# Performance work log

Hardware: AMD Instinct MI355X
Metric: run time of the kernel (lower is better)

Reference implementation:

```python
import jax, jax.numpy as jnp
import numpy as np

# config constants
B, S, H = 4, 2048, 1024
E = 8                 # n_routed_experts
M = 512               # moe_intermediate_size
K = 2                 # num_experts_per_tok
N_SHARED = 2
SM = M * N_SHARED     # shared expert intermediate
G = 64                # gene_size
GE_TEMP = 1.0
ALPHA = 0.001         # aux_loss_alpha
SEQ_AUX = True
NORM_TOPK = True
COS_TEMP = 0.78
CONS_ALPHA = 0.01
LEAKY_SLOPE = 0.01
EPS_COS = 1e-8


def setup_inputs() -> dict:
    key = jax.random.key(0)
    ks = jax.random.split(key, 12)
    sh = 1.0 / np.sqrt(H)
    sm = 1.0 / np.sqrt(M)
    ssm = 1.0 / np.sqrt(SM)
    sg = 1.0 / np.sqrt(G)
    return {
        "hidden_states": jax.random.normal(ks[0], (B, S, H), jnp.float32),
        "g": jax.random.normal(ks[1], (B, G), jnp.float32),
        "wt": jax.random.uniform(ks[2], (E, H), jnp.float32, -sh, sh),   # gate weight_token
        "wg": jax.random.uniform(ks[3], (E, G), jnp.float32, -sg, sg),   # gate weight_gene
        "w_gate": jax.random.uniform(ks[4], (E, H, M), jnp.float32, -sh, sh),
        "w_up": jax.random.uniform(ks[5], (E, H, M), jnp.float32, -sh, sh),
        "w_down": jax.random.uniform(ks[6], (E, M, H), jnp.float32, -sm, sm),
        "sw_gate": jax.random.uniform(ks[7], (H, SM), jnp.float32, -sh, sh),
        "sw_up": jax.random.uniform(ks[8], (H, SM), jnp.float32, -sh, sh),
        "sw_down": jax.random.uniform(ks[9], (SM, H), jnp.float32, -ssm, ssm),
    }


def _leaky(x):
    return jnp.where(x >= 0, x, LEAKY_SLOPE * x)


def _moe_forward(hidden_states, g, wt, wg, w_gate, w_up, w_down, sw_gate, sw_up, sw_down):
    b, s, h = hidden_states.shape
    x = hidden_states.reshape(-1, h)                    # [T, H], T = b*s
    T = x.shape[0]

    # ---- gate ----
    logits_h = x @ wt.T                                 # [T, E]
    logits_g = g @ wg.T                                 # [b, E]
    logits_g = jnp.repeat(logits_g, s, axis=0)          # [T, E]
    logits = (logits_h + logits_g / GE_TEMP) / (1.0 + 1.0 / GE_TEMP)
    scores = jax.nn.softmax(logits, axis=-1)            # [T, E]
    topk_w, topk_idx = jax.lax.top_k(scores, K)         # [T, K]
    if K > 1 and NORM_TOPK:
        topk_w = topk_w / (topk_w.sum(-1, keepdims=True) + 1e-20)

    # aux loss (seq_aux=True)
    onehot = jax.nn.one_hot(topk_idx.reshape(b, s * K), E, dtype=jnp.float32)  # [b, s*K, E]
    ce = onehot.sum(1) / (s * K / E)                    # [b, E]
    aux_loss = (ce * scores.reshape(b, s, E).mean(1)).sum(1).mean() * ALPHA

    # ---- routed experts: dense stacked compute, then gather ----
    gp = _leaky(jnp.einsum('th,ehm->etm', x, w_gate))   # [E, T, M]
    up = jnp.einsum('th,ehm->etm', x, w_up)
    y_all = jnp.einsum('etm,emh->eth', gp * up, w_down) # [E, T, H]
    y_sel = y_all[topk_idx, jnp.arange(T)[:, None], :]  # [T, K, H]
    y = (y_sel * topk_w[..., None]).sum(1).reshape(b, s, h)

    # ---- shared expert ----
    p = (_leaky(hidden_states @ sw_gate) * (hidden_states @ sw_up)) @ sw_down
    y = y + p

    # consistency cosine loss
    num = jnp.sum(y * p, -1)
    den = jnp.maximum(jnp.linalg.norm(y, axis=-1), EPS_COS) * jnp.maximum(jnp.linalg.norm(p, axis=-1), EPS_COS)
    closs = CONS_ALPHA * jnp.mean((num / den) / (1.0 + COS_TEMP))
    return y, aux_loss + closs


def reference(hidden_states, g, wt, wg, w_gate, w_up, w_down, sw_gate, sw_up, sw_down):
    y, _ = _moe_forward(hidden_states, g, wt, wg, w_gate, w_up, w_down, sw_gate, sw_up, sw_down)
    return y
```

## Files before the change

### kernel.cpp

```cpp
#include <hip/hip_runtime.h>
#include <stdint.h>

#define T_TOK 8192
#define H_DIM 1024
#define M_DIM 512
#define SM_DIM 1024
#define E_NUM 8
#define S_SEQ 2048
#define G_DIM 64
#define NASSIGN 16384
#define NSLOT (NASSIGN + E_NUM * 256)
#define MAX_TILES (NASSIGN / 256 + E_NUM)
#define NBLK_PLACE (NASSIGN / 256)

typedef float f32x4 __attribute__((ext_vector_type(4)));
typedef short bf16x8 __attribute__((ext_vector_type(8)));

struct TileDesc { int base; int expert; int nrows; };

#define WAITCNT_VM4 asm volatile("s_waitcnt vmcnt(4)" ::: "memory")
#define WAITCNT_VM3 asm volatile("s_waitcnt vmcnt(3)" ::: "memory")
#define WAITCNT_VM0 asm volatile("s_waitcnt vmcnt(0)" ::: "memory")
#define WAITCNT_LGKM0 asm volatile("s_waitcnt lgkmcnt(0)" ::: "memory")

static __device__ __forceinline__ ushort f2b(float f) {
  union { float f; uint32_t u; } a; a.f = f;
  uint32_t r = a.u + 0x7fffu + ((a.u >> 16) & 1u);
  return (ushort)(r >> 16);
}
static __device__ __forceinline__ float b2f(ushort u) {
  union { uint32_t u; float f; } a; a.u = ((uint32_t)u) << 16;
  return a.f;
}
static __device__ __forceinline__ int imin(int a, int b) { return a < b ? a : b; }

static __device__ __forceinline__ void gll16(const void* g, void* l) {
  __builtin_amdgcn_global_load_lds(
      (const __attribute__((address_space(1))) void*)g,
      (__attribute__((address_space(3))) void*)l, 16, 0, 0);
}
static __device__ __forceinline__ int swz(int row) { return (row >> 1) & 3; }
static __device__ __forceinline__ int xcd_remap(int wg, int nwg) {
  return (wg & 7) * (nwg >> 3) + (wg >> 3);
}

__global__ void cvt_x_kernel(const float* __restrict__ x, ushort* __restrict__ xb) {
  int i = blockIdx.x * 256 + threadIdx.x;
  const float4 v = ((const float4*)x)[i];
  ushort4 o;
  o.x = f2b(v.x); o.y = f2b(v.y); o.z = f2b(v.z); o.w = f2b(v.w);
  ((ushort4*)xb)[i] = o;
}

__global__ void tcvt_kernel(const float* __restrict__ src, ushort* __restrict__ dst, int R, int C) {
  __shared__ float tile[32][33];
  size_t bo = (size_t)blockIdx.z * R * C;
  src += bo; dst += bo;
  int c0 = blockIdx.x * 32, r0 = blockIdx.y * 32;
#pragma unroll
  for (int i = 0; i < 4; ++i)
    tile[threadIdx.y + i * 8][threadIdx.x] =
        src[(size_t)(r0 + threadIdx.y + i * 8) * C + c0 + threadIdx.x];
  __syncthreads();
#pragma unroll
  for (int i = 0; i < 4; ++i)
    dst[(size_t)(c0 + threadIdx.y + i * 8) * R + r0 + threadIdx.x] =
        f2b(tile[threadIdx.x][threadIdx.y + i * 8]);
}

__global__ void lg_kernel(const float* __restrict__ g, const float* __restrict__ wg,
                          float* __restrict__ lg) {
  int tid = threadIdx.x;
  if (tid < 4 * E_NUM) {
    int b = tid >> 3, e = tid & 7;
    float s = 0.f;
    for (int i = 0; i < G_DIM; ++i) s += g[b * G_DIM + i] * wg[e * G_DIM + i];
    lg[tid] = s;
  }
}

__global__ __launch_bounds__(64) void router_kernel(
    const float* __restrict__ x, const float* __restrict__ wt, const float* __restrict__ lg,
    int* __restrict__ tidx, float* __restrict__ tw) {
  int t = blockIdx.x;
  int lane = threadIdx.x;
  const float* xr = x + (size_t)t * H_DIM;
  float a[E_NUM];
#pragma unroll
  for (int e = 0; e < E_NUM; ++e) a[e] = 0.f;
  for (int i = lane; i < H_DIM; i += 64) {
    float xv = xr[i];
#pragma unroll
    for (int e = 0; e < E_NUM; ++e) a[e] += xv * wt[e * H_DIM + i];
  }
#pragma unroll
  for (int e = 0; e < E_NUM; ++e)
    for (int off = 32; off; off >>= 1) a[e] += __shfl_xor(a[e], off, 64);
  if (lane == 0) {
    int b = t / S_SEQ;
    float l[E_NUM];
#pragma unroll
    for (int e = 0; e < E_NUM; ++e) l[e] = 0.5f * (a[e] + lg[b * E_NUM + e]);
    int i1 = 0; float b1 = l[0];
#pragma unroll
    for (int e = 1; e < E_NUM; ++e) if (l[e] > b1) { b1 = l[e]; i1 = e; }
    int i2 = -1; float b2 = -1e30f;
#pragma unroll
    for (int e = 0; e < E_NUM; ++e) if (e != i1 && l[e] > b2) { b2 = l[e]; i2 = e; }
    float e2 = expf(b2 - b1);
    float inv = 1.f / (1.f + e2);
    tidx[t * 2] = i1; tidx[t * 2 + 1] = i2;
    tw[t * 2] = inv;  tw[t * 2 + 1] = e2 * inv;
  }
}

__global__ __launch_bounds__(256) void hist_kernel(const int* __restrict__ tidx,
                                                   int* __restrict__ bcount) {
  __shared__ int h[E_NUM];
  int tid = threadIdx.x;
  if (tid < E_NUM) h[tid] = 0;
  __syncthreads();
  atomicAdd(&h[tidx[blockIdx.x * 256 + tid]], 1);
  __syncthreads();
  if (tid < E_NUM) bcount[blockIdx.x * E_NUM + tid] = h[tid];
}

__global__ __launch_bounds__(64) void scan2_kernel(
    const int* __restrict__ bcount, int* __restrict__ boffs, int* __restrict__ offs,
    TileDesc* __restrict__ desc, int* __restrict__ ndesc) {
  __shared__ int cnt[E_NUM];
  __shared__ int off_s[E_NUM];
  int lane = threadIdx.x;
  if (lane < E_NUM) {
    int s = 0;
    for (int b = 0; b < NBLK_PLACE; ++b) s += bcount[b * E_NUM + lane];
    cnt[lane] = s;
  }
  __syncthreads();
  if (lane == 0) {
    int o = 0, nd = 0;
    for (int e = 0; e < E_NUM; ++e) {
      off_s[e] = o;
      offs[e] = o;
      int n = cnt[e];
      for (int tb = 0; tb < n; tb += 256) {
        desc[nd].base = o + tb; desc[nd].expert = e;
        desc[nd].nrows = imin(n - tb, 256);
        ++nd;
      }
      o += n;
    }
    offs[E_NUM] = o;
    *ndesc = nd;
  }
  __syncthreads();
  if (lane < E_NUM) {
    int run = off_s[lane];
    for (int b = 0; b < NBLK_PLACE; ++b) {
      boffs[b * E_NUM + lane] = run;
      run += bcount[b * E_NUM + lane];
    }
  }
}

__global__ __launch_bounds__(256) void place2_kernel(
    const int* __restrict__ tidx, const int* __restrict__ boffs,
    int* __restrict__ perm, int* __restrict__ slot_of) {
  __shared__ int wcnt[4][E_NUM];
  int tid = threadIdx.x, wv = tid >> 6, lane = tid & 63;
  int i = blockIdx.x * 256 + tid;
  int e = tidx[i];
  unsigned long long lower = (lane == 63) ? 0x7fffffffffffffffull : ((1ull << lane) - 1ull);
  int rank = 0;
#pragma unroll
  for (int ee = 0; ee < E_NUM; ++ee) {
    unsigned long long m = __ballot(e == ee);
    if (e == ee) rank = __popcll(m & lower);
    if (lane == 0) wcnt[wv][ee] = __popcll(m);
  }
  __syncthreads();
  int off = boffs[blockIdx.x * E_NUM + e];
  for (int w = 0; w < wv; ++w) off += wcnt[w][e];
  int pos = off + rank;
  perm[pos] = i >> 1;
  slot_of[i] = pos;
}

template <int DUAL>
static __device__ __forceinline__ void gemm_core(
    const ushort* __restrict__ A, const ushort* __restrict__ B0,
    const ushort* __restrict__ B1, void* __restrict__ Out, int outf32,
    int Kd, int NdOut, int rowbase, int nrows, int n0,
    const int* __restrict__ perm, ushort* Asb, ushort* Bsb) {
  constexpr int BN = DUAL ? 256 : 128;
  constexpr int BSTRIDE = BN * 32;
  int tid = threadIdx.x, wv = tid >> 6, lane = tid & 63;
  int sr = tid >> 2, sc = tid & 3;
  int r1 = sr + 128;

  int ga0 = perm ? perm[rowbase + imin(sr, nrows - 1)] : (rowbase + sr);
  int ga1 = perm ? perm[rowbase + imin(r1, nrows - 1)] : (rowbase + r1);
  const ushort* ap0 = A + (size_t)ga0 * Kd + ((sc ^ swz(sr)) << 3);
  const ushort* ap1 = A + (size_t)ga1 * Kd + ((sc ^ swz(r1)) << 3);
  const ushort* bp0;
  const ushort* bp1 = nullptr;
  if (DUAL) {
    int rb0 = n0 + sr, rb1 = n0 + r1;
    const ushort* s0 = ((rb0 >> 4) & 1) ? B1 : B0;
    const ushort* s1 = ((rb1 >> 4) & 1) ? B1 : B0;
    bp0 = s0 + (size_t)(((rb0 >> 5) << 4) + (rb0 & 15)) * Kd + ((sc ^ swz(sr)) << 3);
    bp1 = s1 + (size_t)(((rb1 >> 5) << 4) + (rb1 & 15)) * Kd + ((sc ^ swz(r1)) << 3);
  } else {
    bp0 = B0 + (size_t)(n0 + sr) * Kd + ((sc ^ swz(sr)) << 3);
  }

  auto stageA = [&](int b) {
    ushort* ad = Asb + b * 8192 + wv * 512;
    gll16(ap0, ad); gll16(ap1, ad + 4096);
    ap0 += 32; ap1 += 32;
  };
  auto stageB = [&](int b) {
    ushort* bd = Bsb + b * BSTRIDE + wv * 512;
    gll16(bp0, bd); bp0 += 32;
    if (DUAL) { gll16(bp1, bd + 4096); bp1 += 32; }
  };

  int wr = wv >> 2, wc = wv & 3;
  int lr = lane & 15, cg = lane >> 4;

  constexpr int NF = DUAL ? 4 : 2;
  f32x4 acc[8][NF];
#pragma unroll
  for (int m = 0; m < 8; ++m)
#pragma unroll
    for (int n = 0; n < NF; ++n) acc[m][n] = (f32x4){0.f, 0.f, 0.f, 0.f};

  int nk = Kd >> 5;
  stageA(0); stageB(0);
  stageA(1); stageB(1);
  if (DUAL) WAITCNT_VM4; else WAITCNT_VM3;
  __builtin_amdgcn_s_barrier();

  for (int kt = 0; kt < nk; ++kt) {
    int b = kt % 3;
    const ushort* abuf = Asb + b * 8192;
    const ushort* bbuf = Bsb + b * BSTRIDE;
    bool pf = (kt + 2 < nk);
    int b2 = (kt + 2) % 3;

    if (DUAL) {
      bf16x8 af[8];
#pragma unroll
      for (int m = 0; m < 8; ++m) {
        int row = wr * 128 + m * 16 + lr;
        af[m] = *(const bf16x8*)(abuf + row * 32 + ((cg ^ swz(row)) << 3));
      }
      bf16x8 bq[2];
#pragma unroll
      for (int n = 0; n < 2; ++n) {
        int row = wc * 64 + n * 16 + lr;
        bq[n] = *(const bf16x8*)(bbuf + row * 32 + ((cg ^ swz(row)) << 3));
      }
      if (pf) stageA(b2);
      __builtin_amdgcn_s_setprio(1);
#pragma unroll
      for (int m = 0; m < 8; ++m) {
        acc[m][0] = __builtin_amdgcn_mfma_f32_16x16x32_bf16(af[m], bq[0], acc[m][0], 0, 0, 0);
        acc[m][1] = __builtin_amdgcn_mfma_f32_16x16x32_bf16(af[m], bq[1], acc[m][1], 0, 0, 0);
      }
      __builtin_amdgcn_s_setprio(0);
      bf16x8 bq2[2];
#pragma unroll
      for (int n = 0; n < 2; ++n) {
        int row = wc * 64 + (n + 2) * 16 + lr;
        bq2[n] = *(const bf16x8*)(bbuf + row * 32 + ((cg ^ swz(row)) << 3));
      }
      if (pf) stageB(b2);
      __builtin_amdgcn_s_setprio(1);
#pragma unroll
      for (int m = 0; m < 8; ++m) {
        acc[m][2] = __builtin_amdgcn_mfma_f32_16x16x32_bf16(af[m], bq2[0], acc[m][2], 0, 0, 0);
        acc[m][3] = __builtin_amdgcn_mfma_f32_16x16x32_bf16(af[m], bq2[1], acc[m][3], 0, 0, 0);
      }
      __builtin_amdgcn_s_setprio(0);
    } else {
      bf16x8 bq[2];
#pragma unroll
      for (int n = 0; n < 2; ++n) {
        int row = wc * 32 + n * 16 + lr;
        bq[n] = *(const bf16x8*)(bbuf + row * 32 + ((cg ^ swz(row)) << 3));
      }
      bf16x8 af[4];
#pragma unroll
      for (int m = 0; m < 4; ++m) {
        int row = wr * 128 + m * 16 + lr;
        af[m] = *(const bf16x8*)(abuf + row * 32 + ((cg ^ swz(row)) << 3));
      }
      if (pf) { stageA(b2); stageB(b2); }
      __builtin_amdgcn_s_setprio(1);
#pragma unroll
      for (int m = 0; m < 4; ++m) {
        acc[m][0] = __builtin_amdgcn_mfma_f32_16x16x32_bf16(af[m], bq[0], acc[m][0], 0, 0, 0);
        acc[m][1] = __builtin_amdgcn_mfma_f32_16x16x32_bf16(af[m], bq[1], acc[m][1], 0, 0, 0);
      }
      __builtin_amdgcn_s_setprio(0);
      bf16x8 af2[4];
#pragma unroll
      for (int m = 0; m < 4; ++m) {
        int row = wr * 128 + (m + 4) * 16 + lr;
        af2[m] = *(const bf16x8*)(abuf + row * 32 + ((cg ^ swz(row)) << 3));
      }
      __builtin_amdgcn_s_setprio(1);
#pragma unroll
      for (int m = 0; m < 4; ++m) {
        acc[m + 4][0] = __builtin_amdgcn_mfma_f32_16x16x32_bf16(af2[m], bq[0], acc[m + 4][0], 0, 0, 0);
        acc[m + 4][1] = __builtin_amdgcn_mfma_f32_16x16x32_bf16(af2[m], bq[1], acc[m + 4][1], 0, 0, 0);
      }
      __builtin_amdgcn_s_setprio(0);
    }
    WAITCNT_LGKM0;
    if (pf) { if (DUAL) WAITCNT_VM4; else WAITCNT_VM3; }
    else WAITCNT_VM0;
    __builtin_amdgcn_s_barrier();
  }

  int rq = cg * 4, cq = lr;
  if (DUAL) {
#pragma unroll
    for (int m = 0; m < 8; ++m)
#pragma unroll
      for (int p = 0; p < 2; ++p)
#pragma unroll
        for (int r = 0; r < 4; ++r) {
          int row = wr * 128 + m * 16 + rq + r;
          if (row < nrows) {
            float gv = acc[m][2 * p][r], uv = acc[m][2 * p + 1][r];
            float hv = (gv >= 0.f ? gv : 0.01f * gv) * uv;
            int col = (n0 >> 1) + wc * 32 + p * 16 + cq;
            ((ushort*)Out)[(size_t)(rowbase + row) * NdOut + col] = f2b(hv);
          }
        }
  } else {
#pragma unroll
    for (int m = 0; m < 8; ++m)
#pragma unroll
      for (int n = 0; n < 2; ++n)
#pragma unroll
        for (int r = 0; r < 4; ++r) {
          int row = wr * 128 + m * 16 + rq + r;
          if (row < nrows) {
            int col = n0 + wc * 32 + n * 16 + cq;
            size_t o = (size_t)(rowbase + row) * NdOut + col;
            if (outf32) ((float*)Out)[o] = acc[m][n][r];
            else ((ushort*)Out)[o] = f2b(acc[m][n][r]);
          }
        }
  }
}

__global__ __launch_bounds__(512) void gemm_dual_all(
    const ushort* __restrict__ xb, const ushort* __restrict__ swg,
    const ushort* __restrict__ swu, ushort* __restrict__ hsh,
    const ushort* __restrict__ wg, const ushort* __restrict__ wu,
    ushort* __restrict__ h_e, const int* __restrict__ perm,
    const TileDesc* __restrict__ desc, const int* __restrict__ ndesc) {
  __shared__ ushort Asb[3 * 8192];
  __shared__ ushort Bsb[3 * 8192];
  int id = xcd_remap(blockIdx.x, gridDim.x);
  if (id < 256) {
    int mt = id >> 3, n0 = (id & 7) * 256;
    gemm_core<1>(xb, swg, swu, hsh, 0, H_DIM, SM_DIM, mt * 256, 256, n0, nullptr, Asb, Bsb);
  } else {
    int rid = id - 256;
    int mt = rid >> 2, n0 = (rid & 3) * 256;
    if (mt >= *ndesc) return;
    TileDesc d = desc[mt];
    size_t wo = (size_t)d.expert * M_DIM * H_DIM;
    gemm_core<1>(xb, wg + wo, wu + wo, h_e, 0, H_DIM, M_DIM, d.base, d.nrows, n0, perm, Asb, Bsb);
  }
}

__global__ __launch_bounds__(512) void gemm_down_all(
    const ushort* __restrict__ hsh, const ushort* __restrict__ swd, float* __restrict__ y,
    const ushort* __restrict__ h_e, const ushort* __restrict__ wd, ushort* __restrict__ ye,
    const TileDesc* __restrict__ desc, const int* __restrict__ ndesc) {
  __shared__ ushort Asb[3 * 8192];
  __shared__ ushort Bsb[3 * 4096];
  int id = xcd_remap(blockIdx.x, gridDim.x);
  if (id < 256) {
    int mt = id >> 3, n0 = (id & 7) * 128;
    gemm_core<0>(hsh, swd, nullptr, (void*)y, 1, SM_DIM, H_DIM, mt * 256, 256, n0, nullptr, Asb, Bsb);
  } else {
    int rid = id - 256;
    int mt = rid >> 3, n0 = (rid & 7) * 128;
    if (mt >= *ndesc) return;
    TileDesc d = desc[mt];
    gemm_core<0>(h_e, wd + (size_t)d.expert * H_DIM * M_DIM, nullptr, (void*)ye, 0,
                 M_DIM, H_DIM, d.base, d.nrows, n0, nullptr, Asb, Bsb);
  }
}

__global__ void final_kernel(float* __restrict__ y, const ushort* __restrict__ ye,
                             const int* __restrict__ slot_of, const float* __restrict__ tw) {
  int i = blockIdx.x * 256 + threadIdx.x;
  int t = i >> 8;
  int c4 = (i & 255) * 4;
  int s0 = slot_of[t * 2], s1 = slot_of[t * 2 + 1];
  float w0 = tw[t * 2], w1 = tw[t * 2 + 1];
  float4 v = ((float4*)y)[i];
  ushort4 a = *(const ushort4*)(ye + (size_t)s0 * H_DIM + c4);
  ushort4 b = *(const ushort4*)(ye + (size_t)s1 * H_DIM + c4);
  v.x += w0 * b2f(a.x) + w1 * b2f(b.x);
  v.y += w0 * b2f(a.y) + w1 * b2f(b.y);
  v.z += w0 * b2f(a.z) + w1 * b2f(b.z);
  v.w += w0 * b2f(a.w) + w1 * b2f(b.w);
  ((float4*)y)[i] = v;
}

extern "C" void kernel_launch(void* const* d_in, const int* in_sizes, int n_in,
                              void* d_out, int out_size, void* d_ws, size_t ws_size,
                              hipStream_t stream) {
  const float* x       = (const float*)d_in[0];
  const float* g       = (const float*)d_in[1];
  const float* wt      = (const float*)d_in[2];
  const float* wg      = (const float*)d_in[3];
  const float* w_gate  = (const float*)d_in[4];
  const float* w_up    = (const float*)d_in[5];
  const float* w_down  = (const float*)d_in[6];
  const float* sw_gate = (const float*)d_in[7];
  const float* sw_up   = (const float*)d_in[8];
  const float* sw_down = (const float*)d_in[9];
  float* y = (float*)d_out;

  char* p = (char*)d_ws;
  auto alloc = [&](size_t bytes) -> char* {
    char* r = p;
    p += (bytes + 255) & ~(size_t)255;
    return r;
  };
  ushort* xb    = (ushort*)alloc((size_t)T_TOK * H_DIM * 2);
  ushort* wg_t  = (ushort*)alloc((size_t)E_NUM * M_DIM * H_DIM * 2);
  ushort* wu_t  = (ushort*)alloc((size_t)E_NUM * M_DIM * H_DIM * 2);
  ushort* wd_t  = (ushort*)alloc((size_t)E_NUM * H_DIM * M_DIM * 2);
  ushort* swg_t = (ushort*)alloc((size_t)SM_DIM * H_DIM * 2);
  ushort* swu_t = (ushort*)alloc((size_t)SM_DIM * H_DIM * 2);
  ushort* swd_t = (ushort*)alloc((size_t)H_DIM * SM_DIM * 2);
  float* lg     = (float*)alloc(4 * E_NUM * 4);
  int* tidx     = (int*)alloc(NASSIGN * 4);
  float* tw     = (float*)alloc(NASSIGN * 4);
  int* bcount   = (int*)alloc(NBLK_PLACE * E_NUM * 4);
  int* boffs    = (int*)alloc(NBLK_PLACE * E_NUM * 4);
  int* offs     = (int*)alloc((E_NUM + 1) * 4);
  int* ndesc    = (int*)alloc(4);
  int* perm     = (int*)alloc(NASSIGN * 4);
  int* slot_of  = (int*)alloc(NASSIGN * 4);
  TileDesc* desc = (TileDesc*)alloc(MAX_TILES * sizeof(TileDesc));
  ushort* h_e   = (ushort*)alloc((size_t)NSLOT * M_DIM * 2);
  ushort* hsh   = (ushort*)alloc((size_t)T_TOK * SM_DIM * 2);
  ushort* ye    = (ushort*)alloc((size_t)NSLOT * H_DIM * 2);
  (void)ws_size; (void)in_sizes; (void)n_in; (void)out_size;

  cvt_x_kernel<<<T_TOK * H_DIM / 4 / 256, 256, 0, stream>>>(x, xb);
  dim3 tb(32, 8);
  tcvt_kernel<<<dim3(M_DIM / 32, H_DIM / 32, E_NUM), tb, 0, stream>>>(w_gate, wg_t, H_DIM, M_DIM);
  tcvt_kernel<<<dim3(M_DIM / 32, H_DIM / 32, E_NUM), tb, 0, stream>>>(w_up, wu_t, H_DIM, M_DIM);
  tcvt_kernel<<<dim3(H_DIM / 32, M_DIM / 32, E_NUM), tb, 0, stream>>>(w_down, wd_t, M_DIM, H_DIM);
  tcvt_kernel<<<dim3(SM_DIM / 32, H_DIM / 32, 1), tb, 0, stream>>>(sw_gate, swg_t, H_DIM, SM_DIM);
  tcvt_kernel<<<dim3(SM_DIM / 32, H_DIM / 32, 1), tb, 0, stream>>>(sw_up, swu_t, H_DIM, SM_DIM);
  tcvt_kernel<<<dim3(H_DIM / 32, SM_DIM / 32, 1), tb, 0, stream>>>(sw_down, swd_t, SM_DIM, H_DIM);

  lg_kernel<<<1, 32, 0, stream>>>(g, wg, lg);
  router_kernel<<<T_TOK, 64, 0, stream>>>(x, wt, lg, tidx, tw);
  hist_kernel<<<NBLK_PLACE, 256, 0, stream>>>(tidx, bcount);
  scan2_kernel<<<1, 64, 0, stream>>>(bcount, boffs, offs, desc, ndesc);
  place2_kernel<<<NBLK_PLACE, 256, 0, stream>>>(tidx, boffs, perm, slot_of);

  gemm_dual_all<<<256 + MAX_TILES * 4, 512, 0, stream>>>(
      xb, swg_t, swu_t, hsh, wg_t, wu_t, h_e, perm, desc, ndesc);
  gemm_down_all<<<256 + MAX_TILES * 8, 512, 0, stream>>>(
      hsh, swd_t, y, h_e, wd_t, ye, desc, ndesc);

  final_kernel<<<T_TOK * H_DIM / 4 / 256, 256, 0, stream>>>(y, ye, slot_of, tw);
}
```

Measured before the change: 233.3 us.

## Rewrite GEMM core as 256x256 tile with BK=64 quadrant-pipelined double buffer

Replaces the triple-buffered BK=32 GEMM core with a double-buffered BK=64 core that splits the 256x256 tile into four 128x128 quadrants. Loads for the next K-step are issued between quadrant MFMA phases, each phase separated by a barrier. The down-projection now also uses 256-wide N tiles, halving its grid and doubling reuse of each A tile. The intent is fewer barriers per unit of K, more compute per load, and better overlap of global-to-LDS traffic. The cost is 128KB of LDS per block, which limits occupancy to one block per CU, plus four barriers per K-step.

After: 222.2 us. -4.7%, faster.

```diff
diff --git a/kernel.cpp b/kernel.cpp
--- a/kernel.cpp
+++ b/kernel.cpp
@@ -18,8 +18,9 @@
 
 struct TileDesc { int base; int expert; int nrows; };
 
+#define WAITCNT_VM6 asm volatile("s_waitcnt vmcnt(6)" ::: "memory")
 #define WAITCNT_VM4 asm volatile("s_waitcnt vmcnt(4)" ::: "memory")
-#define WAITCNT_VM3 asm volatile("s_waitcnt vmcnt(3)" ::: "memory")
+#define WAITCNT_VM2 asm volatile("s_waitcnt vmcnt(2)" ::: "memory")
 #define WAITCNT_VM0 asm volatile("s_waitcnt vmcnt(0)" ::: "memory")
 #define WAITCNT_LGKM0 asm volatile("s_waitcnt lgkmcnt(0)" ::: "memory")
 
@@ -39,7 +40,6 @@
       (const __attribute__((address_space(1))) void*)g,
       (__attribute__((address_space(3))) void*)l, 16, 0, 0);
 }
-static __device__ __forceinline__ int swz(int row) { return (row >> 1) & 3; }
 static __device__ __forceinline__ int xcd_remap(int wg, int nwg) {
   return (wg & 7) * (nwg >> 3) + (wg >> 3);
 }
@@ -187,175 +187,175 @@
 }
 
 template <int DUAL>
-static __device__ __forceinline__ void gemm_core(
+static __device__ __forceinline__ void gemm_core8(
     const ushort* __restrict__ A, const ushort* __restrict__ B0,
     const ushort* __restrict__ B1, void* __restrict__ Out, int outf32,
     int Kd, int NdOut, int rowbase, int nrows, int n0,
-    const int* __restrict__ perm, ushort* Asb, ushort* Bsb) {
-  constexpr int BN = DUAL ? 256 : 128;
-  constexpr int BSTRIDE = BN * 32;
+    const int* __restrict__ perm, ushort* __restrict__ LDS) {
   int tid = threadIdx.x, wv = tid >> 6, lane = tid & 63;
-  int sr = tid >> 2, sc = tid & 3;
-  int r1 = sr + 128;
-
-  int ga0 = perm ? perm[rowbase + imin(sr, nrows - 1)] : (rowbase + sr);
-  int ga1 = perm ? perm[rowbase + imin(r1, nrows - 1)] : (rowbase + r1);
-  const ushort* ap0 = A + (size_t)ga0 * Kd + ((sc ^ swz(sr)) << 3);
-  const ushort* ap1 = A + (size_t)ga1 * Kd + ((sc ^ swz(r1)) << 3);
-  const ushort* bp0;
-  const ushort* bp1 = nullptr;
-  if (DUAL) {
-    int rb0 = n0 + sr, rb1 = n0 + r1;
-    const ushort* s0 = ((rb0 >> 4) & 1) ? B1 : B0;
-    const ushort* s1 = ((rb1 >> 4) & 1) ? B1 : B0;
-    bp0 = s0 + (size_t)(((rb0 >> 5) << 4) + (rb0 & 15)) * Kd + ((sc ^ swz(sr)) << 3);
-    bp1 = s1 + (size_t)(((rb1 >> 5) << 4) + (rb1 & 15)) * Kd + ((sc ^ swz(r1)) << 3);
-  } else {
-    bp0 = B0 + (size_t)(n0 + sr) * Kd + ((sc ^ swz(sr)) << 3);
-  }
-
-  auto stageA = [&](int b) {
-    ushort* ad = Asb + b * 8192 + wv * 512;
-    gll16(ap0, ad); gll16(ap1, ad + 4096);
-    ap0 += 32; ap1 += 32;
-  };
-  auto stageB = [&](int b) {
-    ushort* bd = Bsb + b * BSTRIDE + wv * 512;
-    gll16(bp0, bd); bp0 += 32;
-    if (DUAL) { gll16(bp1, bd + 4096); bp1 += 32; }
-  };
-
   int wr = wv >> 2, wc = wv & 3;
   int lr = lane & 15, cg = lane >> 4;
-
-  constexpr int NF = DUAL ? 4 : 2;
-  f32x4 acc[8][NF];
-#pragma unroll
-  for (int m = 0; m < 8; ++m)
-#pragma unroll
-    for (int n = 0; n < NF; ++n) acc[m][n] = (f32x4){0.f, 0.f, 0.f, 0.f};
-
-  int nk = Kd >> 5;
-  stageA(0); stageB(0);
-  stageA(1); stageB(1);
-  if (DUAL) WAITCNT_VM4; else WAITCNT_VM3;
+  int sid = lane >> 3, dch = lane & 7;
+
+  const ushort* apA[2][2];
+  const ushort* apB[2][2];
+#pragma unroll
+  for (int qm = 0; qm < 2; ++qm)
+#pragma unroll
+    for (int k = 0; k < 2; ++k) {
+      int idx = k * 64 + wv * 8 + sid;
+      int gch = dch ^ (idx & 7);
+      int grow = (idx >> 6) * 128 + qm * 64 + (idx & 63);
+      grow = imin(grow, nrows - 1);
+      int arow = perm ? perm[rowbase + grow] : rowbase + grow;
+      apA[qm][k] = A + (size_t)arow * Kd + gch * 8;
+    }
+#pragma unroll
+  for (int qn = 0; qn < 2; ++qn)
+#pragma unroll
+    for (int k = 0; k < 2; ++k) {
+      int idx = k * 64 + wv * 8 + sid;
+      int gch = dch ^ (idx & 7);
+      int vrow = n0 + (idx >> 5) * 64 + qn * 32 + (idx & 31);
+      const ushort* src; int brow;
+      if (DUAL) {
+        src = ((vrow >> 4) & 1) ? B1 : B0;
+        brow = (vrow >> 5) * 16 + (vrow & 15);
+      } else {
+        src = B0; brow = vrow;
+      }
+      apB[qn][k] = src + (size_t)brow * Kd + gch * 8;
+    }
+
+  auto stgA = [&](int qm, int k, int nd) {
+    gll16(apA[qm][k], LDS + nd * 16384 + qm * 8192 + (k * 512 + wv * 64) * 8);
+    apA[qm][k] += 64;
+  };
+  auto stgB = [&](int qn, int k, int nd) {
+    gll16(apB[qn][k], LDS + 32768 + nd * 16384 + qn * 8192 + (k * 512 + wv * 64) * 8);
+    apB[qn][k] += 64;
+  };
+  auto rdA = [&](int d, int qm, int m, int kk) -> bf16x8 {
+    int idx = wr * 64 + m * 16 + lr;
+    int ch = (kk * 4 + cg) ^ (idx & 7);
+    return *(const bf16x8*)(LDS + d * 16384 + qm * 8192 + idx * 64 + ch * 8);
+  };
+  auto rdB = [&](int d, int qn, int n, int kk) -> bf16x8 {
+    int idx = wc * 32 + n * 16 + lr;
+    int ch = (kk * 4 + cg) ^ (idx & 7);
+    return *(const bf16x8*)(LDS + 32768 + d * 16384 + qn * 8192 + idx * 64 + ch * 8);
+  };
+
+  f32x4 acc[2][2][4][2];
+#pragma unroll
+  for (int qm = 0; qm < 2; ++qm)
+#pragma unroll
+    for (int qn = 0; qn < 2; ++qn)
+#pragma unroll
+      for (int m = 0; m < 4; ++m)
+#pragma unroll
+        for (int n = 0; n < 2; ++n) acc[qm][qn][m][n] = (f32x4){0.f, 0.f, 0.f, 0.f};
+
+  int nk = Kd >> 6;
+  stgA(0, 0, 0); stgA(0, 1, 0);
+  stgB(0, 0, 0); stgB(0, 1, 0);
+  stgB(1, 0, 0); stgB(1, 1, 0);
+  stgA(1, 0, 0); stgA(1, 1, 0);
+  WAITCNT_VM4;
   __builtin_amdgcn_s_barrier();
 
-  for (int kt = 0; kt < nk; ++kt) {
-    int b = kt % 3;
-    const ushort* abuf = Asb + b * 8192;
-    const ushort* bbuf = Bsb + b * BSTRIDE;
-    bool pf = (kt + 2 < nk);
-    int b2 = (kt + 2) % 3;
-
-    if (DUAL) {
-      bf16x8 af[8];
-#pragma unroll
-      for (int m = 0; m < 8; ++m) {
-        int row = wr * 128 + m * 16 + lr;
-        af[m] = *(const bf16x8*)(abuf + row * 32 + ((cg ^ swz(row)) << 3));
-      }
-      bf16x8 bq[2];
+  for (int t = 0; t < nk; ++t) {
+    int cur = t & 1, nxt = cur ^ 1;
+    bool hn = (t + 1 < nk);
+    bf16x8 a0f[4][2], a1f[4][2], b0f[2][2], b1f[2][2];
+
+#pragma unroll
+    for (int m = 0; m < 4; ++m) { a0f[m][0] = rdA(cur, 0, m, 0); a0f[m][1] = rdA(cur, 0, m, 1); }
+#pragma unroll
+    for (int n = 0; n < 2; ++n) { b0f[n][0] = rdB(cur, 0, n, 0); b0f[n][1] = rdB(cur, 0, n, 1); }
+    if (hn) { stgA(0, 0, nxt); stgA(0, 1, nxt); WAITCNT_VM4; } else { WAITCNT_VM2; }
+    WAITCNT_LGKM0;
+    __builtin_amdgcn_s_barrier();
+    __builtin_amdgcn_s_setprio(1);
+#pragma unroll
+    for (int m = 0; m < 4; ++m)
 #pragma unroll
       for (int n = 0; n < 2; ++n) {
-        int row = wc * 64 + n * 16 + lr;
-        bq[n] = *(const bf16x8*)(bbuf + row * 32 + ((cg ^ swz(row)) << 3));
-      }
-      if (pf) stageA(b2);
-      __builtin_amdgcn_s_setprio(1);
-#pragma unroll
-      for (int m = 0; m < 8; ++m) {
-        acc[m][0] = __builtin_amdgcn_mfma_f32_16x16x32_bf16(af[m], bq[0], acc[m][0], 0, 0, 0);
-        acc[m][1] = __builtin_amdgcn_mfma_f32_16x16x32_bf16(af[m], bq[1], acc[m][1], 0, 0, 0);
-      }
-      __builtin_amdgcn_s_setprio(0);
-      bf16x8 bq2[2];
+        acc[0][0][m][n] = __builtin_amdgcn_mfma_f32_16x16x32_bf16(a0f[m][0], b0f[n][0], acc[0][0][m][n], 0, 0, 0);
+        acc[0][0][m][n] = __builtin_amdgcn_mfma_f32_16x16x32_bf16(a0f[m][1], b0f[n][1], acc[0][0][m][n], 0, 0, 0);
+      }
+    __builtin_amdgcn_s_setprio(0);
+
+#pragma unroll
+    for (int n = 0; n < 2; ++n) { b1f[n][0] = rdB(cur, 1, n, 0); b1f[n][1] = rdB(cur, 1, n, 1); }
+    if (hn) { stgB(0, 0, nxt); stgB(0, 1, nxt); WAITCNT_VM4; } else { WAITCNT_VM0; }
+    WAITCNT_LGKM0;
+    __builtin_amdgcn_s_barrier();
+    __builtin_amdgcn_s_setprio(1);
+#pragma unroll
+    for (int m = 0; m < 4; ++m)
 #pragma unroll
       for (int n = 0; n < 2; ++n) {
-        int row = wc * 64 + (n + 2) * 16 + lr;
-        bq2[n] = *(const bf16x8*)(bbuf + row * 32 + ((cg ^ swz(row)) << 3));
-      }
-      if (pf) stageB(b2);
-      __builtin_amdgcn_s_setprio(1);
-#pragma unroll
-      for (int m = 0; m < 8; ++m) {
-        acc[m][2] = __builtin_amdgcn_mfma_f32_16x16x32_bf16(af[m], bq2[0], acc[m][2], 0, 0, 0);
-        acc[m][3] = __builtin_amdgcn_mfma_f32_16x16x32_bf16(af[m], bq2[1], acc[m][3], 0, 0, 0);
-      }
-      __builtin_amdgcn_s_setprio(0);
-    } else {
-      bf16x8 bq[2];
+        acc[0][1][m][n] = __builtin_amdgcn_mfma_f32_16x16x32_bf16(a0f[m][0], b1f[n][0], acc[0][1][m][n], 0, 0, 0);
+        acc[0][1][m][n] = __builtin_amdgcn_mfma_f32_16x16x32_bf16(a0f[m][1], b1f[n][1], acc[0][1][m][n], 0, 0, 0);
+      }
+    __builtin_amdgcn_s_setprio(0);
+
+#pragma unroll
+    for (int m = 0; m < 4; ++m) { a1f[m][0] = rdA(cur, 1, m, 0); a1f[m][1] = rdA(cur, 1, m, 1); }
+    if (hn) { stgB(1, 0, nxt); stgB(1, 1, nxt); WAITCNT_VM6; }
+    WAITCNT_LGKM0;
+    __builtin_amdgcn_s_barrier();
+    __builtin_amdgcn_s_setprio(1);
+#pragma unroll
+    for (int m = 0; m < 4; ++m)
 #pragma unroll
       for (int n = 0; n < 2; ++n) {
-        int row = wc * 32 + n * 16 + lr;
-        bq[n] = *(const bf16x8*)(bbuf + row * 32 + ((cg ^ swz(row)) << 3));
-      }
-      bf16x8 af[4];
-#pragma unroll
-      for (int m = 0; m < 4; ++m) {
-        int row = wr * 128 + m * 16 + lr;
-        af[m] = *(const bf16x8*)(abuf + row * 32 + ((cg ^ swz(row)) << 3));
-      }
-      if (pf) { stageA(b2); stageB(b2); }
-      __builtin_amdgcn_s_setprio(1);
-#pragma unroll
-      for (int m = 0; m < 4; ++m) {
-        acc[m][0] = __builtin_amdgcn_mfma_f32_16x16x32_bf16(af[m], bq[0], acc[m][0], 0, 0, 0);
-        acc[m][1] = __builtin_amdgcn_mfma_f32_16x16x32_bf16(af[m], bq[1], acc[m][1], 0, 0, 0);
-      }
-      __builtin_amdgcn_s_setprio(0);
-      bf16x8 af2[4];
-#pragma unroll
-      for (int m = 0; m < 4; ++m) {
-        int row = wr * 128 + (m + 4) * 16 + lr;
-        af2[m] = *(const bf16x8*)(abuf + row * 32 + ((cg ^ swz(row)) << 3));
-      }
-      __builtin_amdgcn_s_setprio(1);
-#pragma unroll
-      for (int m = 0; m < 4; ++m) {
-        acc[m + 4][0] = __builtin_amdgcn_mfma_f32_16x16x32_bf16(af2[m], bq[0], acc[m + 4][0], 0, 0, 0);
-        acc[m + 4][1] = __builtin_amdgcn_mfma_f32_16x16x32_bf16(af2[m], bq[1], acc[m + 4][1], 0, 0, 0);
-      }
-      __builtin_amdgcn_s_setprio(0);
-    }
+        acc[1][0][m][n] = __builtin_amdgcn_mfma_f32_16x16x32_bf16(a1f[m][0], b0f[n][0], acc[1][0][m][n], 0, 0, 0);
+        acc[1][0][m][n] = __builtin_amdgcn_mfma_f32_16x16x32_bf16(a1f[m][1], b0f[n][1], acc[1][0][m][n], 0, 0, 0);
+      }
+    __builtin_amdgcn_s_setprio(0);
+
+    if (hn) { stgA(1, 0, nxt); stgA(1, 1, nxt); WAITCNT_VM4; }
     WAITCNT_LGKM0;
-    if (pf) { if (DUAL) WAITCNT_VM4; else WAITCNT_VM3; }
-    else WAITCNT_VM0;
     __builtin_amdgcn_s_barrier();
-  }
-
-  int rq = cg * 4, cq = lr;
-  if (DUAL) {
-#pragma unroll
-    for (int m = 0; m < 8; ++m)
-#pragma unroll
-      for (int p = 0; p < 2; ++p)
+    __builtin_amdgcn_s_setprio(1);
+#pragma unroll
+    for (int m = 0; m < 4; ++m)
+#pragma unroll
+      for (int n = 0; n < 2; ++n) {
+        acc[1][1][m][n] = __builtin_amdgcn_mfma_f32_16x16x32_bf16(a1f[m][0], b1f[n][0], acc[1][1][m][n], 0, 0, 0);
+        acc[1][1][m][n] = __builtin_amdgcn_mfma_f32_16x16x32_bf16(a1f[m][1], b1f[n][1], acc[1][1][m][n], 0, 0, 0);
+      }
+    __builtin_amdgcn_s_setprio(0);
+  }
+
+#pragma unroll
+  for (int qm = 0; qm < 2; ++qm)
+#pragma unroll
+    for (int qn = 0; qn < 2; ++qn)
+#pragma unroll
+      for (int m = 0; m < 4; ++m)
 #pragma unroll
         for (int r = 0; r < 4; ++r) {
-          int row = wr * 128 + m * 16 + rq + r;
+          int row = wr * 128 + qm * 64 + m * 16 + cg * 4 + r;
           if (row < nrows) {
-            float gv = acc[m][2 * p][r], uv = acc[m][2 * p + 1][r];
-            float hv = (gv >= 0.f ? gv : 0.01f * gv) * uv;
-            int col = (n0 >> 1) + wc * 32 + p * 16 + cq;
-            ((ushort*)Out)[(size_t)(rowbase + row) * NdOut + col] = f2b(hv);
+            if (DUAL) {
+              float gv = acc[qm][qn][m][0][r], uv = acc[qm][qn][m][1][r];
+              float hv = (gv >= 0.f ? gv : 0.01f * gv) * uv;
+              int col = ((n0 >> 5) + wc * 2 + qn) * 16 + lr;
+              ((ushort*)Out)[(size_t)(rowbase + row) * NdOut + col] = f2b(hv);
+            } else {
+#pragma unroll
+              for (int n = 0; n < 2; ++n) {
+                int col = n0 + wc * 64 + qn * 32 + n * 16 + lr;
+                size_t o = (size_t)(rowbase + row) * NdOut + col;
+                if (outf32) ((float*)Out)[o] = acc[qm][qn][m][n][r];
+                else ((ushort*)Out)[o] = f2b(acc[qm][qn][m][n][r]);
+              }
+            }
           }
         }
-  } else {
-#pragma unroll
-    for (int m = 0; m < 8; ++m)
-#pragma unroll
-      for (int n = 0; n < 2; ++n)
-#pragma unroll
-        for (int r = 0; r < 4; ++r) {
-          int row = wr * 128 + m * 16 + rq + r;
-          if (row < nrows) {
-            int col = n0 + wc * 32 + n * 16 + cq;
-            size_t o = (size_t)(rowbase + row) * NdOut + col;
-            if (outf32) ((float*)Out)[o] = acc[m][n][r];
-            else ((ushort*)Out)[o] = f2b(acc[m][n][r]);
-          }
-        }
-  }
 }
 
 __global__ __launch_bounds__(512) void gemm_dual_all(
@@ -364,19 +364,18 @@
     const ushort* __restrict__ wg, const ushort* __restrict__ wu,
     ushort* __restrict__ h_e, const int* __restrict__ perm,
     const TileDesc* __restrict__ desc, const int* __restrict__ ndesc) {
-  __shared__ ushort Asb[3 * 8192];
-  __shared__ ushort Bsb[3 * 8192];
+  __shared__ ushort LDS[65536];
   int id = xcd_remap(blockIdx.x, gridDim.x);
   if (id < 256) {
     int mt = id >> 3, n0 = (id & 7) * 256;
-    gemm_core<1>(xb, swg, swu, hsh, 0, H_DIM, SM_DIM, mt * 256, 256, n0, nullptr, Asb, Bsb);
+    gemm_core8<1>(xb, swg, swu, hsh, 0, H_DIM, SM_DIM, mt * 256, 256, n0, nullptr, LDS);
   } else {
     int rid = id - 256;
     int mt = rid >> 2, n0 = (rid & 3) * 256;
     if (mt >= *ndesc) return;
     TileDesc d = desc[mt];
     size_t wo = (size_t)d.expert * M_DIM * H_DIM;
-    gemm_core<1>(xb, wg + wo, wu + wo, h_e, 0, H_DIM, M_DIM, d.base, d.nrows, n0, perm, Asb, Bsb);
+    gemm_core8<1>(xb, wg + wo, wu + wo, h_e, 0, H_DIM, M_DIM, d.base, d.nrows, n0, perm, LDS);
   }
 }
 
@@ -384,19 +383,18 @@
     const ushort* __restrict__ hsh, const ushort* __restrict__ swd, float* __restrict__ y,
     const ushort* __restrict__ h_e, const ushort* __restrict__ wd, ushort* __restrict__ ye,
     const TileDesc* __restrict__ desc, const int* __restrict__ ndesc) {
-  __shared__ ushort Asb[3 * 8192];
-  __shared__ ushort Bsb[3 * 4096];
+  __shared__ ushort LDS[65536];
   int id = xcd_remap(blockIdx.x, gridDim.x);
-  if (id < 256) {
-    int mt = id >> 3, n0 = (id & 7) * 128;
-    gemm_core<0>(hsh, swd, nullptr, (void*)y, 1, SM_DIM, H_DIM, mt * 256, 256, n0, nullptr, Asb, Bsb);
+  if (id < 128) {
+    int mt = id >> 2, n0 = (id & 3) * 256;
+    gemm_core8<0>(hsh, swd, nullptr, (void*)y, 1, SM_DIM, H_DIM, mt * 256, 256, n0, nullptr, LDS);
   } else {
-    int rid = id - 256;
-    int mt = rid >> 3, n0 = (rid & 7) * 128;
+    int rid = id - 128;
+    int mt = rid >> 2, n0 = (rid & 3) * 256;
     if (mt >= *ndesc) return;
     TileDesc d = desc[mt];
-    gemm_core<0>(h_e, wd + (size_t)d.expert * H_DIM * M_DIM, nullptr, (void*)ye, 0,
-                 M_DIM, H_DIM, d.base, d.nrows, n0, nullptr, Asb, Bsb);
+    gemm_core8<0>(h_e, wd + (size_t)d.expert * H_DIM * M_DIM, nullptr, (void*)ye, 0,
+                  M_DIM, H_DIM, d.base, d.nrows, n0, nullptr, LDS);
   }
 }
 
@@ -477,7 +475,7 @@
 
   gemm_dual_all<<<256 + MAX_TILES * 4, 512, 0, stream>>>(
       xb, swg_t, swu_t, hsh, wg_t, wu_t, h_e, perm, desc, ndesc);
-  gemm_down_all<<<256 + MAX_TILES * 8, 512, 0, stream>>>(
+  gemm_down_all<<<128 + MAX_TILES * 4, 512, 0, stream>>>(
       hsh, swd_t, y, h_e, wd_t, ye, desc, ndesc);
 
   final_kernel<<<T_TOK * H_DIM / 4 / 256, 256, 0, stream>>>(y, ye, slot_of, tw);
```
